# Performance work log

Hardware: AMD Instinct MI355X
Metric: run time of the kernel (lower is better)

Reference implementation:

```python
import jax, jax.numpy as jnp
import numpy as np
import math

B, T, S, C, W = 32, 512, 128, 30, 10  # batch, seq, spans, candidates, max span width
D_CTX, D_ENT, H, V = 768, 300, 100, 200000
EPS = 1e-5
NEG = -1e30


def layer_norm(x, g, b):
    mu = jnp.mean(x, axis=-1, keepdims=True)
    var = jnp.mean((x - mu) ** 2, axis=-1, keepdims=True)
    return (x - mu) / jnp.sqrt(var + EPS) * g + b


def setup_inputs() -> dict:
    key = jax.random.key(0)
    ks = jax.random.split(key, 12)
    contextual_embeddings = jax.random.normal(ks[0], (B, T, D_CTX), jnp.float32)
    mask = jnp.ones((B, T), jnp.int32)
    starts = jax.random.randint(ks[1], (B, S), 0, T - W)
    widths = jax.random.randint(ks[2], (B, S), 0, W)
    ends = starts + widths  # inclusive end, AllenNLP convention
    # pad last 8 spans per example with -1 to exercise span masking
    pad = jnp.arange(S)[None, :] >= S - 8
    starts = jnp.where(pad, -1, starts)
    ends = jnp.where(pad, -1, ends)
    candidate_spans = jnp.stack([starts, ends], axis=-1)
    candidate_entities = jax.random.randint(ks[3], (B, S, C), 1, V)
    pri = jax.random.uniform(ks[4], (B, S, C), jnp.float32)
    candidate_entity_priors = pri / pri.sum(-1, keepdims=True)
    candidate_segment_ids = jnp.zeros((B, S, C), jnp.int32)
    # parameters
    entity_table = jax.random.normal(ks[5], (V, D_ENT), jnp.float32) * 0.02
    proj_W = jax.random.normal(ks[6], (D_ENT, D_CTX), jnp.float32) * 0.02
    proj_b = jnp.zeros((D_ENT,), jnp.float32)
    kg_g = jnp.ones((D_ENT,), jnp.float32)
    kg_b = jnp.zeros((D_ENT,), jnp.float32)
    ln_g = jnp.ones((D_ENT,), jnp.float32)
    ln_b = jnp.zeros((D_ENT,), jnp.float32)
    attn_W = jax.random.normal(ks[7], (1, D_ENT), jnp.float32) * 0.02
    attn_b = jnp.zeros((1,), jnp.float32)
    W1 = jax.random.normal(ks[8], (H, 2), jnp.float32) * 0.02
    b1 = jnp.zeros((H,), jnp.float32)
    W2 = jax.random.normal(ks[9], (1, H), jnp.float32) * 0.02
    b2 = jnp.zeros((1,), jnp.float32)
    return dict(contextual_embeddings=contextual_embeddings, mask=mask,
                candidate_spans=candidate_spans, candidate_entities=candidate_entities,
                candidate_entity_priors=candidate_entity_priors,
                candidate_segment_ids=candidate_segment_ids,
                entity_table=entity_table, proj_W=proj_W, proj_b=proj_b,
                kg_g=kg_g, kg_b=kg_b, ln_g=ln_g, ln_b=ln_b,
                attn_W=attn_W, attn_b=attn_b, W1=W1, b1=b1, W2=W2, b2=b2)


def reference(contextual_embeddings, mask, candidate_spans, candidate_entities,
              candidate_entity_priors, candidate_segment_ids, entity_table,
              proj_W, proj_b, kg_g, kg_b, ln_g, ln_b, attn_W, attn_b,
              W1, b1, W2, b2):
    # --- entity embedding lookup + KG layer norm ---
    ent_emb = layer_norm(entity_table[candidate_entities], kg_g, kg_b)  # (B,S,C,D)

    # --- bert -> kg projection ---
    proj = contextual_embeddings @ proj_W.T + proj_b  # (B,T,D_ENT)

    span_mask = candidate_spans[:, :, 0] > -1  # (B,S)

    # --- SelfAttentiveSpanExtractor ---
    att_logits = (proj @ attn_W.T + attn_b)[..., 0]  # (B,T)
    starts = candidate_spans[..., 0]
    ends = candidate_spans[..., 1]
    widths = ends - starts
    offs = jnp.arange(W)  # max span width
    idx = starts[..., None] + offs  # (B,S,W)
    valid = (offs <= widths[..., None]) & (idx >= 0) & (idx < T)
    idx_c = jnp.where(valid, idx, 0)
    idx_flat = idx_c.reshape(B, S * W)
    span_emb = jnp.take_along_axis(proj, idx_flat[..., None], axis=1).reshape(B, S, W, D_ENT)
    span_log = jnp.take_along_axis(att_logits, idx_flat, axis=1).reshape(B, S, W)
    attn = jax.nn.softmax(jnp.where(valid, span_log, NEG), axis=-1)  # (B,S,W)
    span_rep = jnp.einsum('bsw,bswd->bsd', attn, span_emb)
    span_rep = span_rep * span_mask[..., None].astype(span_rep.dtype)
    span_rep = layer_norm(span_rep, ln_g, ln_b)  # (B,S,D)

    # --- DotAttentionWithPrior ---
    scores = jnp.einsum('bsd,bscd->bsc', span_rep, ent_emb) / math.sqrt(D_ENT)
    feat = jnp.stack([scores, candidate_entity_priors], axis=-1)  # (B,S,C,2)
    h = jax.nn.relu(feat @ W1.T + b1)
    link = (h @ W2.T + b2)[..., 0]  # (B,S,C)
    entity_mask = candidate_entities > 0
    linking_scores = jnp.where(entity_mask, link, -10000.0)
    normed = jax.nn.softmax(linking_scores, axis=-1)
    weighted = jnp.einsum('bsc,bscd->bsd', normed, ent_emb)
    return linking_scores, weighted
```

## Files before the change

kernel.cpp:

```cpp
#include <hip/hip_runtime.h>
#include <hip/hip_bf16.h>
#include <math.h>

#define BB 32
#define TT 512
#define SS 128
#define CC 30
#define WW 10
#define DCTX 768
#define DENT 300
#define HH 100
#define EPSF 1e-5f
#define NEGF -1e30f

typedef __attribute__((ext_vector_type(8))) short bf16x8;
typedef __attribute__((ext_vector_type(4))) float f32x4;

#define NK  (DCTX / 32)
#define NCT 20

template<int C, int M>
__device__ __forceinline__ float dppadd(float x) {
    union { float f; int i; } u, r;
    u.f = x;
    r.i = __builtin_amdgcn_update_dpp(0, u.i, C, M, 0xf, true);
    return x + r.f;
}
__device__ __forceinline__ float wave_red(float x) {
    x = dppadd<0x111, 0xf>(x);
    x = dppadd<0x112, 0xf>(x);
    x = dppadd<0x114, 0xf>(x);
    x = dppadd<0x118, 0xf>(x);
    x = dppadd<0x142, 0xa>(x);
    x = dppadd<0x143, 0xc>(x);
    union { float f; int i; } u; u.f = x;
    u.i = __builtin_amdgcn_readlane(u.i, 63);
    return u.f;
}

__device__ __forceinline__ void dma16(const float* g, float* l) {
    __builtin_amdgcn_global_load_lds(
        (const __attribute__((address_space(1))) void*)g,
        (__attribute__((address_space(3))) void*)l, 16, 0, 0);
}

__device__ __forceinline__ ushort f2bf(float f) {
    __hip_bfloat16 h = __float2bfloat16(f);
    return *reinterpret_cast<ushort*>(&h);
}

__device__ __forceinline__ float dot4(float4 a, float4 b) {
    return a.x*b.x + a.y*b.y + a.z*b.z + a.w*b.w;
}
__device__ __forceinline__ float hadd8(float4 a, float4 b) {
    return a.x+a.y+a.z+a.w + b.x+b.y+b.z+b.w;
}
__device__ __forceinline__ ushort4 cvt4(float4 v) {
    ushort4 h; h.x = f2bf(v.x); h.y = f2bf(v.y); h.z = f2bf(v.z); h.w = f2bf(v.w);
    return h;
}

__global__ __launch_bounds__(256) void wpre_kernel(
    const float* __restrict__ Wt, ushort* __restrict__ wpre)
{
    const int g = blockIdx.x * 256 + threadIdx.x;
    const int l = g & 63;
    const int t = (g >> 6) % NK;
    const int ct = g / (NK * 64);
    const int col = ct * 16 + (l & 15);
    const int k = t * 32 + (l >> 4) * 8;
    ushort4 h0 = {0, 0, 0, 0}, h1 = {0, 0, 0, 0};
    if (col < DENT) {
        h0 = cvt4(*(const float4*)(Wt + (size_t)col * DCTX + k));
        h1 = cvt4(*(const float4*)(Wt + (size_t)col * DCTX + k + 4));
    }
    *(ushort4*)(wpre + (size_t)g * 8)     = h0;
    *(ushort4*)(wpre + (size_t)g * 8 + 4) = h1;
}

#define GBM 64
#define LDA 40

__global__ __launch_bounds__(512) void gemm_proj_mfma(
    const float*  __restrict__ A,
    const ushort* __restrict__ wpre,
    const float*  __restrict__ bias,
    float* __restrict__ out)
{
    __shared__ ushort Al[2][GBM * LDA];
    const int tid = threadIdx.x;
    const int lane = tid & 63;
    const int wv = tid >> 6;
    const int wm = wv >> 2;
    const int wn = wv & 3;
    const int m0 = blockIdx.x * GBM;
    const int ar = tid >> 3;
    const int ak = (tid & 7) * 4;
    const int lr = lane & 15;
    const int kq = (lane >> 4) * 8;

    const float* aP = A + (size_t)(m0 + ar) * DCTX + ak;
    const ushort* bp = wpre + (size_t)wn * 5 * NK * 512 + (size_t)lane * 8;

    f32x4 acc[2][5];
    #pragma unroll
    for (int i = 0; i < 2; ++i)
        #pragma unroll
        for (int j = 0; j < 5; ++j)
            acc[i][j] = (f32x4){0.f, 0.f, 0.f, 0.f};

    bf16x8 cb[5], nb[5];
    #pragma unroll
    for (int j = 0; j < 5; ++j)
        cb[j] = *(const bf16x8*)(bp + (size_t)j * NK * 512);

#define STOREA(BUF, v_) (*(ushort4*)&Al[BUF][ar * LDA + ak] = cvt4(v_))

#define COMPUTE(BUF) do {                                                      \
        bf16x8 af_[2];                                                         \
        _Pragma("unroll")                                                      \
        for (int i_ = 0; i_ < 2; ++i_)                                         \
            af_[i_] = *(const bf16x8*)&Al[BUF][(wm*32 + i_*16 + lr)*LDA + kq]; \
        _Pragma("unroll")                                                      \
        for (int j_ = 0; j_ < 5; ++j_)                                         \
            acc[0][j_] = __builtin_amdgcn_mfma_f32_16x16x32_bf16(              \
                af_[0], cb[j_], acc[0][j_], 0, 0, 0);                          \
        _Pragma("unroll")                                                      \
        for (int j_ = 0; j_ < 5; ++j_)                                         \
            acc[1][j_] = __builtin_amdgcn_mfma_f32_16x16x32_bf16(              \
                af_[1], cb[j_], acc[1][j_], 0, 0, 0);                          \
    } while (0)

    float4 avA = *(const float4*)(aP);
    float4 avB = *(const float4*)(aP + 32);
    STOREA(0, avA);
    __syncthreads();

    #pragma unroll 1
    for (int kk = 0; kk < NK; kk += 2) {
        #pragma unroll
        for (int j = 0; j < 5; ++j)
            nb[j] = *(const bf16x8*)(bp + ((size_t)j * NK + kk + 1) * 512);
        if (kk + 2 < NK) avA = *(const float4*)(aP + (kk + 2) * 32);
        COMPUTE(0);
        STOREA(1, avB);
        __syncthreads();
        #pragma unroll
        for (int j = 0; j < 5; ++j) cb[j] = nb[j];
        if (kk + 2 < NK) {
            #pragma unroll
            for (int j = 0; j < 5; ++j)
                nb[j] = *(const bf16x8*)(bp + ((size_t)j * NK + kk + 2) * 512);
            avB = *(const float4*)(aP + (kk + 3) * 32);
        }
        COMPUTE(1);
        if (kk + 2 < NK) STOREA(0, avA);
        __syncthreads();
        #pragma unroll
        for (int j = 0; j < 5; ++j) cb[j] = nb[j];
    }

    const int lq = lane >> 4;
    #pragma unroll
    for (int j = 0; j < 5; ++j) {
        int col = wn * 80 + j * 16 + lr;
        if (col < DENT) {
            float bv = bias[col];
            #pragma unroll
            for (int i = 0; i < 2; ++i)
                #pragma unroll
                for (int r = 0; r < 4; ++r) {
                    int row = m0 + wm * 32 + i * 16 + lq * 4 + r;
                    out[(size_t)row * DENT + col] = acc[i][j][r] + bv;
                }
        }
    }
}

__global__ __launch_bounds__(256) void span_kernel(
    const float* __restrict__ proj,
    const int*   __restrict__ spans,
    const float* __restrict__ attn_W,
    const float* __restrict__ attn_b,
    const float* __restrict__ ln_g,
    const float* __restrict__ ln_b,
    const float* __restrict__ kg_g,
    const float* __restrict__ kg_b,
    float* __restrict__ srg_out,
    float* __restrict__ sgsb)
{
    const int bs = blockIdx.x * 4 + (threadIdx.x >> 6);
    const int b = bs >> 7;
    const int lane = threadIdx.x & 63;
    const int start = spans[bs * 2 + 0];
    const int end   = spans[bs * 2 + 1];
    const int width = end - start;
    const bool lo = lane < 11;
    const float4 z = make_float4(0.f, 0.f, 0.f, 0.f);

    const float4* attW4 = (const float4*)attn_W;
    float4 w0 = attW4[lane];
    float4 w1 = lo ? attW4[64 + lane] : z;

    float4 a0[WW], a1[WW];
    float slog[WW];
    bool vld[WW];
    #pragma unroll
    for (int w = 0; w < WW; ++w) {
        int idx = start + w;
        vld[w] = (w <= width) && (idx >= 0) && (idx < TT);
        const float4* pr = (const float4*)(proj + (size_t)(b * TT + (vld[w] ? idx : 0)) * DENT);
        a0[w] = pr[lane];
        a1[w] = lo ? pr[64 + lane] : z;
        slog[w] = dot4(a0[w], w0) + dot4(a1[w], w1);
    }
    const float ab = attn_b[0];
    #pragma unroll
    for (int w = 0; w < WW; ++w) {
        float r = wave_red(slog[w]);
        slog[w] = vld[w] ? r + ab : NEGF;
    }
    float m = slog[0];
    #pragma unroll
    for (int w = 1; w < WW; ++w) m = fmaxf(m, slog[w]);
    float den = 0.f;
    float aw[WW];
    #pragma unroll
    for (int w = 0; w < WW; ++w) { aw[w] = expf(slog[w] - m); den += aw[w]; }
    const float inv = 1.f / den;
    const float msk = (start > -1) ? inv : 0.f;

    float4 acc0 = z, acc1 = z;
    #pragma unroll
    for (int w = 0; w < WW; ++w) {
        float c = aw[w] * msk;
        acc0.x = fmaf(c, a0[w].x, acc0.x); acc0.y = fmaf(c, a0[w].y, acc0.y);
        acc0.z = fmaf(c, a0[w].z, acc0.z); acc0.w = fmaf(c, a0[w].w, acc0.w);
        acc1.x = fmaf(c, a1[w].x, acc1.x); acc1.y = fmaf(c, a1[w].y, acc1.y);
        acc1.z = fmaf(c, a1[w].z, acc1.z); acc1.w = fmaf(c, a1[w].w, acc1.w);
    }
    float s1 = wave_red(hadd8(acc0, acc1));
    float s2 = wave_red(dot4(acc0, acc0) + dot4(acc1, acc1));
    const float mu = s1 * (1.f / DENT);
    const float rstd = rsqrtf(s2 * (1.f / DENT) - mu * mu + EPSF);

    const float4* lg4 = (const float4*)ln_g;  const float4* lb4 = (const float4*)ln_b;
    const float4* gg4 = (const float4*)kg_g;  const float4* gb4 = (const float4*)kg_b;
    float pg = 0.f, pb = 0.f;
    float4* so = (float4*)(srg_out + (size_t)bs * DENT);
    {
        float4 g = lg4[lane], bb_ = lb4[lane], gg = gg4[lane], gb = gb4[lane];
        float4 val;
        val.x = fmaf((acc0.x - mu) * rstd, g.x, bb_.x);
        val.y = fmaf((acc0.y - mu) * rstd, g.y, bb_.y);
        val.z = fmaf((acc0.z - mu) * rstd, g.z, bb_.z);
        val.w = fmaf((acc0.w - mu) * rstd, g.w, bb_.w);
        float4 vg = make_float4(val.x * gg.x, val.y * gg.y, val.z * gg.z, val.w * gg.w);
        so[lane] = vg;
        pg += vg.x + vg.y + vg.z + vg.w;
        pb += val.x * gb.x + val.y * gb.y + val.z * gb.z + val.w * gb.w;
    }
    if (lo) {
        float4 g = lg4[64 + lane], bb_ = lb4[64 + lane], gg = gg4[64 + lane], gb = gb4[64 + lane];
        float4 val;
        val.x = fmaf((acc1.x - mu) * rstd, g.x, bb_.x);
        val.y = fmaf((acc1.y - mu) * rstd, g.y, bb_.y);
        val.z = fmaf((acc1.z - mu) * rstd, g.z, bb_.z);
        val.w = fmaf((acc1.w - mu) * rstd, g.w, bb_.w);
        float4 vg = make_float4(val.x * gg.x, val.y * gg.y, val.z * gg.z, val.w * gg.w);
        so[64 + lane] = vg;
        pg += vg.x + vg.y + vg.z + vg.w;
        pb += val.x * gb.x + val.y * gb.y + val.z * gb.z + val.w * gb.w;
    }
    pg = wave_red(pg);
    pb = wave_red(pb);
    if (lane == 0) { sgsb[bs * 2 + 0] = pg; sgsb[bs * 2 + 1] = pb; }
}

__global__ __launch_bounds__(512, 8) void final_fused(
    const float* __restrict__ srg,
    const float* __restrict__ sgsb,
    const int*   __restrict__ cand,
    const float* __restrict__ priors,
    const float* __restrict__ table,
    const float* __restrict__ W1,
    const float* __restrict__ b1,
    const float* __restrict__ W2,
    const float* __restrict__ b2,
    const float* __restrict__ kg_g,
    const float* __restrict__ kg_b,
    float* __restrict__ out_link,
    float* __restrict__ out_w)
{
    __shared__ float rows[CC][DENT];
    __shared__ float smu[CC], srs[CC], ssc[CC], sexp[CC];
    const int bs = blockIdx.x;
    const int tid = threadIdx.x;
    const int lane = tid & 63;
    const int wv = tid >> 6;
    const bool lo = lane < 11;
    const float4 z = make_float4(0.f, 0.f, 0.f, 0.f);

    int es[4] = {0, 0, 0, 0};
    #pragma unroll
    for (int k = 0; k < 4; ++k) {
        int c = wv + k * 8;
        if (c < CC) {
            int e = cand[bs * CC + c];
            es[k] = e;
            const float* src = table + (size_t)e * DENT;
            dma16(src + lane * 4, &rows[c][0]);
            if (lo) dma16(src + 256 + lane * 4, &rows[c][256]);
        }
    }

    const float4* sg4 = (const float4*)(srg + (size_t)bs * DENT);
    float4 g0 = sg4[lane];
    float4 g1 = lo ? sg4[64 + lane] : z;
    const float SG = sgsb[bs * 2 + 0];
    const float SB = sgsb[bs * 2 + 1];
    const float W1a0 = W1[2 * lane], W1b0 = W1[2 * lane + 1];
    const float B10 = b1[lane], W20 = W2[lane];
    float W1a1 = 0.f, W1b1 = 0.f, B11 = 0.f, W21 = 0.f;
    if (lane < HH - 64) {
        int j = lane + 64;
        W1a1 = W1[2 * j]; W1b1 = W1[2 * j + 1]; B11 = b1[j]; W21 = W2[j];
    }
    const float b2v = b2[0];
    const float isd = rsqrtf((float)DENT);

    __syncthreads();

    #pragma unroll
    for (int k = 0; k < 4; ++k) {
        int c = wv + k * 8;
        if (c < CC) {
            float4 xa = *(const float4*)&rows[c][lane * 4];
            float4 xb = lo ? *(const float4*)&rows[c][256 + lane * 4] : z;
            float s1 = wave_red(hadd8(xa, xb));
            float s2 = wave_red(dot4(xa, xa) + dot4(xb, xb));
            float s3 = wave_red(dot4(g0, xa) + dot4(g1, xb));
            float mu = s1 * (1.f / DENT);
            float rstd = rsqrtf(s2 * (1.f / DENT) - mu * mu + EPSF);
            float score = (rstd * (s3 - mu * SG) + SB) * isd;
            float pr = priors[bs * CC + c];
            float h  = fmaxf(fmaf(W1a0, score, fmaf(W1b0, pr, B10)), 0.f);
            float h2 = fmaxf(fmaf(W1a1, score, fmaf(W1b1, pr, B11)), 0.f);
            float lp = wave_red(fmaf(W21, h2, W20 * h)) + b2v;
            float link = (es[k] > 0) ? lp : -10000.0f;
            if (lane == 0) {
                smu[c] = mu; srs[c] = rstd; ssc[c] = link;
                out_link[bs * CC + c] = link;
            }
        }
    }
    __syncthreads();

    if (tid < CC) {
        float m = ssc[0];
        #pragma unroll
        for (int c = 1; c < CC; ++c) m = fmaxf(m, ssc[c]);
        sexp[tid] = expf(ssc[tid] - m);
    }
    __syncthreads();

    const int d = tid;
    if (d < DENT) {
        float den = 0.f;
        #pragma unroll
        for (int c = 0; c < CC; ++c) den += sexp[c];
        const float inv = 1.f / den;
        float acc = 0.f, S2 = 0.f, sn = 0.f;
        #pragma unroll
        for (int c = 0; c < CC; ++c) {
            float n = sexp[c] * inv;
            float coef = n * srs[c];
            acc = fmaf(coef, rows[c][d], acc);
            S2 = fmaf(coef, smu[c], S2);
            sn += n;
        }
        out_w[(size_t)bs * DENT + d] = kg_g[d] * (acc - S2) + kg_b[d] * sn;
    }
}

extern "C" void kernel_launch(void* const* d_in, const int* in_sizes, int n_in,
                              void* d_out, int out_size, void* d_ws, size_t ws_size,
                              hipStream_t stream) {
    const float* ctx    = (const float*)d_in[0];
    const int*   spans  = (const int*)d_in[2];
    const int*   cand   = (const int*)d_in[3];
    const float* priors = (const float*)d_in[4];
    const float* table  = (const float*)d_in[6];
    const float* projW  = (const float*)d_in[7];
    const float* projb  = (const float*)d_in[8];
    const float* kg_g   = (const float*)d_in[9];
    const float* kg_b   = (const float*)d_in[10];
    const float* ln_g   = (const float*)d_in[11];
    const float* ln_b   = (const float*)d_in[12];
    const float* attW   = (const float*)d_in[13];
    const float* attb   = (const float*)d_in[14];
    const float* W1     = (const float*)d_in[15];
    const float* b1     = (const float*)d_in[16];
    const float* W2     = (const float*)d_in[17];
    const float* b2     = (const float*)d_in[18];

    float* proj = (float*)d_ws;
    float* srg  = proj + (size_t)BB * TT * DENT;
    float* sgsb = srg + (size_t)BB * SS * DENT;
    ushort* wpre = (ushort*)srg;

    float* out_link = (float*)d_out;
    float* out_w    = out_link + (size_t)BB * SS * CC;

    wpre_kernel<<<NCT * NK * 64 / 256, 256, 0, stream>>>(projW, wpre);
    gemm_proj_mfma<<<BB * TT / GBM, 512, 0, stream>>>(ctx, wpre, projb, proj);
    span_kernel<<<BB * SS / 4, 256, 0, stream>>>(proj, spans, attW, attb,
                                                 ln_g, ln_b, kg_g, kg_b, srg, sgsb);
    final_fused<<<BB * SS, 512, 0, stream>>>(srg, sgsb, cand, priors, table,
                                             W1, b1, W2, b2, kg_g, kg_b,
                                             out_link, out_w);
}
```

Measured before the change: 81.96 us.

## Fuse span attention and layer norm into the final linking kernel

Merges span_kernel into the final kernel. Each block now DMAs its span's projected rows into LDS, computes the attention softmax, weighted sum and layer norm with block-level reductions, and keeps the gated span representation in shared memory. This drops one launch and the global write/read of the srg and sgsb intermediates. In exchange it adds LDS use (about 12KB for prow), extra barriers and cross-wave reductions, and the candidate-row gather now overlaps with the span work.

```diff
diff --git a/kernel.cpp b/kernel.cpp
--- a/kernel.cpp
+++ b/kernel.cpp
@@ -48,7 +48,6 @@
     __hip_bfloat16 h = __float2bfloat16(f);
     return *reinterpret_cast<ushort*>(&h);
 }
-
 __device__ __forceinline__ float dot4(float4 a, float4 b) {
     return a.x*b.x + a.y*b.y + a.z*b.z + a.w*b.w;
 }
@@ -177,109 +176,15 @@
     }
 }
 
-__global__ __launch_bounds__(256) void span_kernel(
+__global__ __launch_bounds__(512) void final2(
     const float* __restrict__ proj,
     const int*   __restrict__ spans,
-    const float* __restrict__ attn_W,
-    const float* __restrict__ attn_b,
+    const float* __restrict__ attW,
+    const float* __restrict__ attb,
     const float* __restrict__ ln_g,
     const float* __restrict__ ln_b,
     const float* __restrict__ kg_g,
     const float* __restrict__ kg_b,
-    float* __restrict__ srg_out,
-    float* __restrict__ sgsb)
-{
-    const int bs = blockIdx.x * 4 + (threadIdx.x >> 6);
-    const int b = bs >> 7;
-    const int lane = threadIdx.x & 63;
-    const int start = spans[bs * 2 + 0];
-    const int end   = spans[bs * 2 + 1];
-    const int width = end - start;
-    const bool lo = lane < 11;
-    const float4 z = make_float4(0.f, 0.f, 0.f, 0.f);
-
-    const float4* attW4 = (const float4*)attn_W;
-    float4 w0 = attW4[lane];
-    float4 w1 = lo ? attW4[64 + lane] : z;
-
-    float4 a0[WW], a1[WW];
-    float slog[WW];
-    bool vld[WW];
-    #pragma unroll
-    for (int w = 0; w < WW; ++w) {
-        int idx = start + w;
-        vld[w] = (w <= width) && (idx >= 0) && (idx < TT);
-        const float4* pr = (const float4*)(proj + (size_t)(b * TT + (vld[w] ? idx : 0)) * DENT);
-        a0[w] = pr[lane];
-        a1[w] = lo ? pr[64 + lane] : z;
-        slog[w] = dot4(a0[w], w0) + dot4(a1[w], w1);
-    }
-    const float ab = attn_b[0];
-    #pragma unroll
-    for (int w = 0; w < WW; ++w) {
-        float r = wave_red(slog[w]);
-        slog[w] = vld[w] ? r + ab : NEGF;
-    }
-    float m = slog[0];
-    #pragma unroll
-    for (int w = 1; w < WW; ++w) m = fmaxf(m, slog[w]);
-    float den = 0.f;
-    float aw[WW];
-    #pragma unroll
-    for (int w = 0; w < WW; ++w) { aw[w] = expf(slog[w] - m); den += aw[w]; }
-    const float inv = 1.f / den;
-    const float msk = (start > -1) ? inv : 0.f;
-
-    float4 acc0 = z, acc1 = z;
-    #pragma unroll
-    for (int w = 0; w < WW; ++w) {
-        float c = aw[w] * msk;
-        acc0.x = fmaf(c, a0[w].x, acc0.x); acc0.y = fmaf(c, a0[w].y, acc0.y);
-        acc0.z = fmaf(c, a0[w].z, acc0.z); acc0.w = fmaf(c, a0[w].w, acc0.w);
-        acc1.x = fmaf(c, a1[w].x, acc1.x); acc1.y = fmaf(c, a1[w].y, acc1.y);
-        acc1.z = fmaf(c, a1[w].z, acc1.z); acc1.w = fmaf(c, a1[w].w, acc1.w);
-    }
-    float s1 = wave_red(hadd8(acc0, acc1));
-    float s2 = wave_red(dot4(acc0, acc0) + dot4(acc1, acc1));
-    const float mu = s1 * (1.f / DENT);
-    const float rstd = rsqrtf(s2 * (1.f / DENT) - mu * mu + EPSF);
-
-    const float4* lg4 = (const float4*)ln_g;  const float4* lb4 = (const float4*)ln_b;
-    const float4* gg4 = (const float4*)kg_g;  const float4* gb4 = (const float4*)kg_b;
-    float pg = 0.f, pb = 0.f;
-    float4* so = (float4*)(srg_out + (size_t)bs * DENT);
-    {
-        float4 g = lg4[lane], bb_ = lb4[lane], gg = gg4[lane], gb = gb4[lane];
-        float4 val;
-        val.x = fmaf((acc0.x - mu) * rstd, g.x, bb_.x);
-        val.y = fmaf((acc0.y - mu) * rstd, g.y, bb_.y);
-        val.z = fmaf((acc0.z - mu) * rstd, g.z, bb_.z);
-        val.w = fmaf((acc0.w - mu) * rstd, g.w, bb_.w);
-        float4 vg = make_float4(val.x * gg.x, val.y * gg.y, val.z * gg.z, val.w * gg.w);
-        so[lane] = vg;
-        pg += vg.x + vg.y + vg.z + vg.w;
-        pb += val.x * gb.x + val.y * gb.y + val.z * gb.z + val.w * gb.w;
-    }
-    if (lo) {
-        float4 g = lg4[64 + lane], bb_ = lb4[64 + lane], gg = gg4[64 + lane], gb = gb4[64 + lane];
-        float4 val;
-        val.x = fmaf((acc1.x - mu) * rstd, g.x, bb_.x);
-        val.y = fmaf((acc1.y - mu) * rstd, g.y, bb_.y);
-        val.z = fmaf((acc1.z - mu) * rstd, g.z, bb_.z);
-        val.w = fmaf((acc1.w - mu) * rstd, g.w, bb_.w);
-        float4 vg = make_float4(val.x * gg.x, val.y * gg.y, val.z * gg.z, val.w * gg.w);
-        so[64 + lane] = vg;
-        pg += vg.x + vg.y + vg.z + vg.w;
-        pb += val.x * gb.x + val.y * gb.y + val.z * gb.z + val.w * gb.w;
-    }
-    pg = wave_red(pg);
-    pb = wave_red(pb);
-    if (lane == 0) { sgsb[bs * 2 + 0] = pg; sgsb[bs * 2 + 1] = pb; }
-}
-
-__global__ __launch_bounds__(512, 8) void final_fused(
-    const float* __restrict__ srg,
-    const float* __restrict__ sgsb,
     const int*   __restrict__ cand,
     const float* __restrict__ priors,
     const float* __restrict__ table,
@@ -287,38 +192,57 @@
     const float* __restrict__ b1,
     const float* __restrict__ W2,
     const float* __restrict__ b2,
-    const float* __restrict__ kg_g,
-    const float* __restrict__ kg_b,
     float* __restrict__ out_link,
     float* __restrict__ out_w)
 {
-    __shared__ float rows[CC][DENT];
+    __shared__ __align__(16) float rows[CC][DENT];
+    __shared__ __align__(16) float prow[WW][DENT];
+    __shared__ __align__(16) float srg_s[DENT];
+    __shared__ float slog_s[WW];
     __shared__ float smu[CC], srs[CC], ssc[CC], sexp[CC];
+    __shared__ float2 wpartA[8], wpartB[8];
     const int bs = blockIdx.x;
+    const int b = bs >> 7;
     const int tid = threadIdx.x;
     const int lane = tid & 63;
     const int wv = tid >> 6;
     const bool lo = lane < 11;
     const float4 z = make_float4(0.f, 0.f, 0.f, 0.f);
 
+    const int start = spans[bs * 2 + 0];
+    const int end   = spans[bs * 2 + 1];
+    const int width = end - start;
+
+    #pragma unroll
+    for (int k = 0; k < 2; ++k) {
+        int r = wv + k * 8;
+        if (r < WW) {
+            int idx = start + r;
+            bool v = (r <= width) && (idx >= 0) && (idx < TT);
+            const float* src = proj + (size_t)(b * TT + (v ? idx : 0)) * DENT;
+            dma16(src + lane * 4, &prow[r][0]);
+            if (lo) dma16(src + 256 + lane * 4, &prow[r][256]);
+        }
+    }
     int es[4] = {0, 0, 0, 0};
+    float prv[4] = {0.f, 0.f, 0.f, 0.f};
     #pragma unroll
     for (int k = 0; k < 4; ++k) {
         int c = wv + k * 8;
         if (c < CC) {
             int e = cand[bs * CC + c];
             es[k] = e;
+            prv[k] = priors[bs * CC + c];
             const float* src = table + (size_t)e * DENT;
             dma16(src + lane * 4, &rows[c][0]);
             if (lo) dma16(src + 256 + lane * 4, &rows[c][256]);
         }
     }
 
-    const float4* sg4 = (const float4*)(srg + (size_t)bs * DENT);
-    float4 g0 = sg4[lane];
-    float4 g1 = lo ? sg4[64 + lane] : z;
-    const float SG = sgsb[bs * 2 + 0];
-    const float SB = sgsb[bs * 2 + 1];
+    const float4* attW4 = (const float4*)attW;
+    float4 w0 = attW4[lane];
+    float4 w1 = lo ? attW4[64 + lane] : z;
+    const float ab = attb[0];
     const float W1a0 = W1[2 * lane], W1b0 = W1[2 * lane + 1];
     const float B10 = b1[lane], W20 = W2[lane];
     float W1a1 = 0.f, W1b1 = 0.f, B11 = 0.f, W21 = 0.f;
@@ -328,24 +252,86 @@
     }
     const float b2v = b2[0];
     const float isd = rsqrtf((float)DENT);
-
-    __syncthreads();
-
+    float lg = 0.f, lb = 0.f, gg = 0.f, gb = 0.f;
+    if (tid < DENT) { lg = ln_g[tid]; lb = ln_b[tid]; gg = kg_g[tid]; gb = kg_b[tid]; }
+
+    __syncthreads();
+
+    #pragma unroll
+    for (int k = 0; k < 2; ++k) {
+        int r = wv + k * 8;
+        if (r < WW) {
+            int idx = start + r;
+            bool v = (r <= width) && (idx >= 0) && (idx < TT);
+            float4 a0 = *(const float4*)&prow[r][lane * 4];
+            float4 a1 = lo ? *(const float4*)&prow[r][256 + lane * 4] : z;
+            float lgt = wave_red(dot4(a0, w0) + dot4(a1, w1));
+            if (lane == 0) slog_s[r] = v ? lgt + ab : NEGF;
+        }
+    }
+    __syncthreads();
+
+    float aw[WW];
+    {
+        float m = slog_s[0];
+        #pragma unroll
+        for (int w = 1; w < WW; ++w) m = fmaxf(m, slog_s[w]);
+        float den = 0.f;
+        #pragma unroll
+        for (int w = 0; w < WW; ++w) { aw[w] = expf(slog_s[w] - m); den += aw[w]; }
+        const float msk = (start > -1) ? (1.f / den) : 0.f;
+        #pragma unroll
+        for (int w = 0; w < WW; ++w) aw[w] *= msk;
+    }
+    float acc = 0.f;
+    if (tid < DENT) {
+        #pragma unroll
+        for (int w = 0; w < WW; ++w) acc = fmaf(aw[w], prow[w][tid], acc);
+    }
+    {
+        float s1p = wave_red(acc);
+        float s2p = wave_red(acc * acc);
+        if (lane == 0) wpartA[wv] = make_float2(s1p, s2p);
+    }
+    __syncthreads();
+    float s1 = 0.f, s2 = 0.f;
+    #pragma unroll
+    for (int i = 0; i < 8; ++i) { s1 += wpartA[i].x; s2 += wpartA[i].y; }
+    const float mu_s = s1 * (1.f / DENT);
+    const float rstd_s = rsqrtf(s2 * (1.f / DENT) - mu_s * mu_s + EPSF);
+    float val = 0.f, vg = 0.f, pbp = 0.f;
+    if (tid < DENT) {
+        val = fmaf((acc - mu_s) * rstd_s, lg, lb);
+        vg = val * gg;
+        srg_s[tid] = vg;
+        pbp = val * gb;
+    }
+    {
+        float pgp = wave_red(vg);
+        float pbq = wave_red(pbp);
+        if (lane == 0) wpartB[wv] = make_float2(pgp, pbq);
+    }
+    __syncthreads();
+    float SG = 0.f, SB = 0.f;
+    #pragma unroll
+    for (int i = 0; i < 8; ++i) { SG += wpartB[i].x; SB += wpartB[i].y; }
+
+    float4 g0 = *(const float4*)&srg_s[lane * 4];
+    float4 g1 = lo ? *(const float4*)&srg_s[256 + lane * 4] : z;
     #pragma unroll
     for (int k = 0; k < 4; ++k) {
         int c = wv + k * 8;
         if (c < CC) {
             float4 xa = *(const float4*)&rows[c][lane * 4];
             float4 xb = lo ? *(const float4*)&rows[c][256 + lane * 4] : z;
-            float s1 = wave_red(hadd8(xa, xb));
-            float s2 = wave_red(dot4(xa, xa) + dot4(xb, xb));
-            float s3 = wave_red(dot4(g0, xa) + dot4(g1, xb));
-            float mu = s1 * (1.f / DENT);
-            float rstd = rsqrtf(s2 * (1.f / DENT) - mu * mu + EPSF);
-            float score = (rstd * (s3 - mu * SG) + SB) * isd;
-            float pr = priors[bs * CC + c];
-            float h  = fmaxf(fmaf(W1a0, score, fmaf(W1b0, pr, B10)), 0.f);
-            float h2 = fmaxf(fmaf(W1a1, score, fmaf(W1b1, pr, B11)), 0.f);
+            float c1 = wave_red(hadd8(xa, xb));
+            float c2 = wave_red(dot4(xa, xa) + dot4(xb, xb));
+            float c3 = wave_red(dot4(g0, xa) + dot4(g1, xb));
+            float mu = c1 * (1.f / DENT);
+            float rstd = rsqrtf(c2 * (1.f / DENT) - mu * mu + EPSF);
+            float score = (rstd * (c3 - mu * SG) + SB) * isd;
+            float h  = fmaxf(fmaf(W1a0, score, fmaf(W1b0, prv[k], B10)), 0.f);
+            float h2 = fmaxf(fmaf(W1a1, score, fmaf(W1b1, prv[k], B11)), 0.f);
             float lp = wave_red(fmaf(W21, h2, W20 * h)) + b2v;
             float link = (es[k] > 0) ? lp : -10000.0f;
             if (lane == 0) {
@@ -364,22 +350,21 @@
     }
     __syncthreads();
 
-    const int d = tid;
-    if (d < DENT) {
+    if (tid < DENT) {
         float den = 0.f;
         #pragma unroll
         for (int c = 0; c < CC; ++c) den += sexp[c];
         const float inv = 1.f / den;
-        float acc = 0.f, S2 = 0.f, sn = 0.f;
+        float a2 = 0.f, S2 = 0.f, sn = 0.f;
         #pragma unroll
         for (int c = 0; c < CC; ++c) {
             float n = sexp[c] * inv;
             float coef = n * srs[c];
-            acc = fmaf(coef, rows[c][d], acc);
+            a2 = fmaf(coef, rows[c][tid], a2);
             S2 = fmaf(coef, smu[c], S2);
             sn += n;
         }
-        out_w[(size_t)bs * DENT + d] = kg_g[d] * (acc - S2) + kg_b[d] * sn;
+        out_w[(size_t)bs * DENT + tid] = gg * (a2 - S2) + gb * sn;
     }
 }
 
@@ -404,19 +389,17 @@
     const float* W2     = (const float*)d_in[17];
     const float* b2     = (const float*)d_in[18];
 
-    float* proj = (float*)d_ws;
-    float* srg  = proj + (size_t)BB * TT * DENT;
-    float* sgsb = srg + (size_t)BB * SS * DENT;
-    ushort* wpre = (ushort*)srg;
+    float*  proj = (float*)d_ws;
+    ushort* wpre = (ushort*)(proj + (size_t)BB * TT * DENT);
 
     float* out_link = (float*)d_out;
     float* out_w    = out_link + (size_t)BB * SS * CC;
 
     wpre_kernel<<<NCT * NK * 64 / 256, 256, 0, stream>>>(projW, wpre);
     gemm_proj_mfma<<<BB * TT / GBM, 512, 0, stream>>>(ctx, wpre, projb, proj);
-    span_kernel<<<BB * SS / 4, 256, 0, stream>>>(proj, spans, attW, attb,
-                                                 ln_g, ln_b, kg_g, kg_b, srg, sgsb);
-    final_fused<<<BB * SS, 512, 0, stream>>>(srg, sgsb, cand, priors, table,
-                                             W1, b1, W2, b2, kg_g, kg_b,
-                                             out_link, out_w);
-}
+    final2<<<BB * SS, 512, 0, stream>>>(proj, spans, attW, attb,
+                                        ln_g, ln_b, kg_g, kg_b,
+                                        cand, priors, table,
+                                        W1, b1, W2, b2,
+                                        out_link, out_w);
+}
```

Measured after the change: 86.17 us. 1.05x slower.
